# Kernel optimization log

Measured on AMD Instinct MI355X. Metric: run time of the kernel, lower is better.

The kernel has to match this reference:

```python
import jax, jax.numpy as jnp
import numpy as np

MACRO_CURVE_ORDER = 3
MAX_ACTION_LEN = 24
NUM_CURVES = 8
VOCAB = 361
NUM_LAYERS = 6
HID = 32


def setup_inputs() -> dict:
    key = jax.random.key(0)
    ks = iter(jax.random.split(key, 32))
    B, N_PART, P, CTX = 4096, 100, 64, 64

    def lin(k, din, dout):
        k1, k2 = jax.random.split(k)
        s = 1.0 / np.sqrt(din)
        return (jax.random.uniform(k1, (din, dout), jnp.float32, -s, s),
                jax.random.uniform(k2, (dout,), jnp.float32, -s, s))

    fc1_w, fc1_b = lin(next(ks), P, 256)
    fc2_w, fc2_b = lin(next(ks), 256, 256)
    fc3_w, fc3_b = lin(next(ks), CTX + 256, 512)
    fc4_w, fc4_b = lin(next(ks), 512, 256)
    fc5_w, fc5_b = lin(next(ks), 256, 128)
    fc6_w, fc6_b = lin(next(ks), 128, 32)
    fc10_w, fc10_b = lin(next(ks), HID, VOCAB)

    s = 1.0 / np.sqrt(HID)
    lstm_wih = jax.random.uniform(next(ks), (NUM_LAYERS, HID, 4 * HID), jnp.float32, -s, s)
    lstm_whh = jax.random.uniform(next(ks), (NUM_LAYERS, HID, 4 * HID), jnp.float32, -s, s)
    lstm_bih = jax.random.uniform(next(ks), (NUM_LAYERS, 4 * HID), jnp.float32, -s, s)
    lstm_bhh = jax.random.uniform(next(ks), (NUM_LAYERS, 4 * HID), jnp.float32, -s, s)

    return {
        "c": jax.random.normal(next(ks), (B, CTX), jnp.float32),
        "x": jax.random.normal(next(ks), (B, N_PART * P), jnp.float32),
        "hidden": jnp.zeros((NUM_LAYERS, B, HID), jnp.float32),
        "cell": jnp.zeros((NUM_LAYERS, B, HID), jnp.float32),
        "fc1_w": fc1_w, "fc1_b": fc1_b, "fc2_w": fc2_w, "fc2_b": fc2_b,
        "fc3_w": fc3_w, "fc3_b": fc3_b, "fc4_w": fc4_w, "fc4_b": fc4_b,
        "fc5_w": fc5_w, "fc5_b": fc5_b, "fc6_w": fc6_w, "fc6_b": fc6_b,
        "lstm_wih": lstm_wih, "lstm_whh": lstm_whh,
        "lstm_bih": lstm_bih, "lstm_bhh": lstm_bhh,
        "fc10_w": fc10_w, "fc10_b": fc10_b,
        "particle_size": P,
    }


def _lstm_stack(x, h, c, wih, whh, bih, bhh):
    """One time step through 6 stacked LSTM layers (PyTorch cell math)."""
    hs, cs = [], []
    inp = x
    for l in range(NUM_LAYERS):
        gates = inp @ wih[l] + bih[l] + h[l] @ whh[l] + bhh[l]  # (B, 4*HID)
        i, f, g, o = jnp.split(gates, 4, axis=-1)
        i, f, o = jax.nn.sigmoid(i), jax.nn.sigmoid(f), jax.nn.sigmoid(o)
        g = jnp.tanh(g)
        c_new = f * c[l] + i * g
        h_new = o * jnp.tanh(c_new)
        hs.append(h_new)
        cs.append(c_new)
        inp = h_new
    return inp, jnp.stack(hs), jnp.stack(cs)


def reference(c, x, hidden, cell, fc1_w, fc1_b, fc2_w, fc2_b, fc3_w, fc3_b,
              fc4_w, fc4_b, fc5_w, fc5_b, fc6_w, fc6_b,
              lstm_wih, lstm_whh, lstm_bih, lstm_bhh, fc10_w, fc10_b,
              particle_size):
    B = x.shape[0]
    # Belief (particle) encoder with mean pooling.
    xp = x.reshape(B, -1, particle_size)
    xp = jax.nn.relu(xp @ fc1_w + fc1_b)
    xp = jax.nn.relu(xp @ fc2_w + fc2_b)
    xp = xp.mean(axis=-2)  # (B, 256)
    z = jnp.concatenate([c, xp], axis=-1)
    z = jax.nn.relu(z @ fc3_w + fc3_b)
    z = jax.nn.relu(z @ fc4_w + fc4_b)
    z = jax.nn.relu(z @ fc5_w + fc5_b)
    z = jax.nn.relu(z @ fc6_w + fc6_b)  # (B, 32)

    def step(carry, _):
        xt, h, cst = carry
        xt, h, cst = _lstm_stack(xt, h, cst, lstm_wih, lstm_whh, lstm_bih, lstm_bhh)
        logits = xt @ fc10_w + fc10_b  # (B, VOCAB)
        idx = jax.lax.top_k(logits, NUM_CURVES)[1]  # (B, NUM_CURVES)
        return (xt, h, cst), idx

    (_, _, _), idxs = jax.lax.scan(step, (z, hidden, cell), None, length=MAX_ACTION_LEN)
    # (T, B, K) -> (B, T*K)
    preds = jnp.transpose(idxs, (1, 0, 2)).reshape(B, MAX_ACTION_LEN * NUM_CURVES)
    return preds
```

## Files before the change

### kernel.cpp

```cpp
#include <hip/hip_runtime.h>
#include <math.h>

#define BATCH 4096
#define NPART 100
#define PSZ   64

__device__ __forceinline__ void fma4(float4& d, const float s, const float4 v) {
    d.x = fmaf(s, v.x, d.x); d.y = fmaf(s, v.y, d.y);
    d.z = fmaf(s, v.z, d.z); d.w = fmaf(s, v.w, d.w);
}
__device__ __forceinline__ float4 addrelu4(const float4 a, const float4 b) {
    return make_float4(fmaxf(a.x + b.x, 0.f), fmaxf(a.y + b.y, 0.f),
                       fmaxf(a.z + b.z, 0.f), fmaxf(a.w + b.w, 0.f));
}

typedef const __attribute__((address_space(1))) unsigned int  gu32;
typedef __attribute__((address_space(3)))       unsigned int  lu32;
__device__ __forceinline__ void gload_lds16(const float* g, float* l) {
    __builtin_amdgcn_global_load_lds((gu32*)g, (lu32*)l, 16, 0, 0);
}

__device__ __forceinline__ void stage_panel(const float* __restrict__ w2,
                                            float* dst, const int p,
                                            const int wv, const int lane) {
    const float* g = w2 + p * (16 * 256) + wv * 256 + lane * 4;
    float*       l = dst + wv * 256;
    #pragma unroll
    for (int s = 0; s < 4; ++s)
        gload_lds16(g + s * 1024, l + s * 1024);
}

__global__ __launch_bounds__(256) void k_tw(
    const float* __restrict__ wih, const float* __restrict__ whh,
    const float* __restrict__ w10,
    float* __restrict__ wtih, float* __restrict__ wthh,
    float* __restrict__ w10t)
{
    const int i = blockIdx.x * 256 + threadIdx.x;
    if (i < 6 * 4096) {
        const int l = i >> 12, r = i & 4095;
        const int g = r >> 5,  k = r & 31;
        wtih[i] = wih[l * 4096 + k * 128 + g];
        wthh[i] = whh[l * 4096 + k * 128 + g];
    }
    if (i < 361 * 32) {
        const int v = i >> 5, k = i & 31;
        w10t[i] = w10[k * 361 + v];
    }
}

template<int NRR>
__device__ __forceinline__ void enc_chunk(
    const float* __restrict__ xb, const int rbase,
    const float* __restrict__ w1c, const float* __restrict__ w2,
    float* __restrict__ h1s, float* __restrict__ wpan,
    const int wv, const int lane, const int rg, const int col0,
    const float4 b1a, const float4 b1b, const float4 b2a, const float4 b2b,
    float* msum)
{
    stage_panel(w2, wpan, 0, wv, lane);

    int rowr[NRR];
    #pragma unroll
    for (int rr = 0; rr < NRR; ++rr)
        rowr[rr] = rbase + ((NRR == 1 && rg >= 4) ? 0 : (rg + 8 * rr));

    float4 a0[NRR], a1[NRR];
    #pragma unroll
    for (int rr = 0; rr < NRR; ++rr) {
        a0[rr] = make_float4(0.f, 0.f, 0.f, 0.f);
        a1[rr] = make_float4(0.f, 0.f, 0.f, 0.f);
    }
    #pragma unroll 2
    for (int k0 = 0; k0 < 64; k0 += 4) {
        float4 bva[4], bvb[4];
        #pragma unroll
        for (int kk = 0; kk < 4; ++kk) {
            bva[kk] = *(const float4*)(w1c + (k0 + kk) * 256);
            bvb[kk] = *(const float4*)(w1c + (k0 + kk) * 256 + 4);
        }
        #pragma unroll
        for (int rr = 0; rr < NRR; ++rr) {
            const float4 av = *(const float4*)(xb + (size_t)rowr[rr] * 64 + k0);
            fma4(a0[rr], av.x, bva[0]); fma4(a0[rr], av.y, bva[1]);
            fma4(a0[rr], av.z, bva[2]); fma4(a0[rr], av.w, bva[3]);
            fma4(a1[rr], av.x, bvb[0]); fma4(a1[rr], av.y, bvb[1]);
            fma4(a1[rr], av.z, bvb[2]); fma4(a1[rr], av.w, bvb[3]);
        }
    }
    #pragma unroll
    for (int rr = 0; rr < NRR; ++rr) {
        const int r = rg + 8 * rr;
        *(float4*)&h1s[r * 260 + col0]     = addrelu4(a0[rr], b1a);
        *(float4*)&h1s[r * 260 + col0 + 4] = addrelu4(a1[rr], b1b);
    }
    __syncthreads();

    float4 c0[NRR], c1[NRR];
    #pragma unroll
    for (int rr = 0; rr < NRR; ++rr) {
        c0[rr] = make_float4(0.f, 0.f, 0.f, 0.f);
        c1[rr] = make_float4(0.f, 0.f, 0.f, 0.f);
    }
    #pragma unroll 1
    for (int p = 0; p < 16; ++p) {
        if (p < 15)
            stage_panel(w2, wpan + ((p + 1) & 1) * (16 * 256), p + 1, wv, lane);
        const float* wp = wpan + (p & 1) * (16 * 256);
        #pragma unroll
        for (int it = 0; it < 4; ++it) {
            const int kk0 = it * 4;
            float4 bva[4], bvb[4];
            #pragma unroll
            for (int kk = 0; kk < 4; ++kk) {
                bva[kk] = *(const float4*)&wp[(kk0 + kk) * 256 + col0];
                bvb[kk] = *(const float4*)&wp[(kk0 + kk) * 256 + col0 + 4];
            }
            const int kg = p * 16 + kk0;
            #pragma unroll
            for (int rr = 0; rr < NRR; ++rr) {
                const float4 av = *(const float4*)&h1s[(rg + 8 * rr) * 260 + kg];
                fma4(c0[rr], av.x, bva[0]); fma4(c0[rr], av.y, bva[1]);
                fma4(c0[rr], av.z, bva[2]); fma4(c0[rr], av.w, bva[3]);
                fma4(c1[rr], av.x, bvb[0]); fma4(c1[rr], av.y, bvb[1]);
                fma4(c1[rr], av.z, bvb[2]); fma4(c1[rr], av.w, bvb[3]);
            }
        }
        __syncthreads();
    }

    #pragma unroll
    for (int rr = 0; rr < NRR; ++rr) {
        if (NRR == 4 || rg < 4) {
            msum[0] += fmaxf(c0[rr].x + b2a.x, 0.f);
            msum[1] += fmaxf(c0[rr].y + b2a.y, 0.f);
            msum[2] += fmaxf(c0[rr].z + b2a.z, 0.f);
            msum[3] += fmaxf(c0[rr].w + b2a.w, 0.f);
            msum[4] += fmaxf(c1[rr].x + b2b.x, 0.f);
            msum[5] += fmaxf(c1[rr].y + b2b.y, 0.f);
            msum[6] += fmaxf(c1[rr].z + b2b.z, 0.f);
            msum[7] += fmaxf(c1[rr].w + b2b.w, 0.f);
        }
    }
}

__global__ __launch_bounds__(256) void k_encoder(
    const float* __restrict__ x,
    const float* __restrict__ w1, const float* __restrict__ b1,
    const float* __restrict__ w2, const float* __restrict__ b2,
    float* __restrict__ xp)
{
    __shared__ __align__(16) float h1s[32 * 260];
    __shared__ __align__(16) float wpan[2 * 16 * 256];
    const int tid  = threadIdx.x;
    const int b    = blockIdx.x;
    const int lane = tid & 63;
    const int wv   = tid >> 6;
    const int cgw  = lane & 7;
    const int rg   = lane >> 3;
    const int col0 = wv * 64 + cgw * 8;

    const float* xb  = x + (size_t)b * (NPART * PSZ);
    const float* w1c = w1 + col0;
    const float4 b1a = *(const float4*)&b1[col0];
    const float4 b1b = *(const float4*)&b1[col0 + 4];
    const float4 b2a = *(const float4*)&b2[col0];
    const float4 b2b = *(const float4*)&b2[col0 + 4];

    float msum[8] = {0.f,0.f,0.f,0.f,0.f,0.f,0.f,0.f};

    enc_chunk<4>(xb,  0, w1c, w2, h1s, wpan, wv, lane, rg, col0, b1a, b1b, b2a, b2b, msum);
    enc_chunk<4>(xb, 32, w1c, w2, h1s, wpan, wv, lane, rg, col0, b1a, b1b, b2a, b2b, msum);
    enc_chunk<4>(xb, 64, w1c, w2, h1s, wpan, wv, lane, rg, col0, b1a, b1b, b2a, b2b, msum);
    enc_chunk<1>(xb, 96, w1c, w2, h1s, wpan, wv, lane, rg, col0, b1a, b1b, b2a, b2b, msum);

    #pragma unroll
    for (int q = 0; q < 8; ++q) {
        msum[q] += __shfl_xor(msum[q], 8, 64);
        msum[q] += __shfl_xor(msum[q], 16, 64);
        msum[q] += __shfl_xor(msum[q], 32, 64);
    }
    if (rg == 0) {
        float4 o0 = make_float4(msum[0] / 100.f, msum[1] / 100.f,
                                msum[2] / 100.f, msum[3] / 100.f);
        float4 o1 = make_float4(msum[4] / 100.f, msum[5] / 100.f,
                                msum[6] / 100.f, msum[7] / 100.f);
        *(float4*)&xp[(size_t)b * 256 + col0]     = o0;
        *(float4*)&xp[(size_t)b * 256 + col0 + 4] = o1;
    }
}

__global__ __launch_bounds__(256) void k_mlp(
    const float* __restrict__ cin, const float* __restrict__ xp,
    const float* __restrict__ w3, const float* __restrict__ b3,
    const float* __restrict__ w4, const float* __restrict__ b4,
    const float* __restrict__ w5, const float* __restrict__ b5,
    const float* __restrict__ w6, const float* __restrict__ b6,
    float* __restrict__ z)
{
    __shared__ float in0[8][320];
    __shared__ float h3[8][512];
    __shared__ float h4[8][256];
    __shared__ float h5[8][128];
    const int tid  = threadIdx.x;
    const int row0 = blockIdx.x * 8;

    for (int i = tid; i < 8 * 16; i += 256) {
        int r = i >> 4, q = i & 15;
        *(float4*)&in0[r][q * 4] = *(const float4*)&cin[(size_t)(row0 + r) * 64 + q * 4];
    }
    for (int i = tid; i < 8 * 64; i += 256) {
        int r = i >> 6, q = i & 63;
        *(float4*)&in0[r][64 + q * 4] = *(const float4*)&xp[(size_t)(row0 + r) * 256 + q * 4];
    }
    __syncthreads();

    {
        float a0[8], a1[8];
        #pragma unroll
        for (int r = 0; r < 8; ++r) { a0[r] = 0.f; a1[r] = 0.f; }
        const int c0 = tid, c1 = tid + 256;
        for (int kq = 0; kq < 80; ++kq) {
            const int k0 = kq * 4;
            float wa0 = w3[(k0+0)*512 + c0], wa1 = w3[(k0+1)*512 + c0];
            float wa2 = w3[(k0+2)*512 + c0], wa3 = w3[(k0+3)*512 + c0];
            float wb0 = w3[(k0+0)*512 + c1], wb1 = w3[(k0+1)*512 + c1];
            float wb2 = w3[(k0+2)*512 + c1], wb3 = w3[(k0+3)*512 + c1];
            #pragma unroll
            for (int r = 0; r < 8; ++r) {
                const float4 a = *(const float4*)&in0[r][k0];
                a0[r] = fmaf(a.x, wa0, fmaf(a.y, wa1, fmaf(a.z, wa2, fmaf(a.w, wa3, a0[r]))));
                a1[r] = fmaf(a.x, wb0, fmaf(a.y, wb1, fmaf(a.z, wb2, fmaf(a.w, wb3, a1[r]))));
            }
        }
        const float bb0 = b3[c0], bb1 = b3[c1];
        #pragma unroll
        for (int r = 0; r < 8; ++r) {
            h3[r][c0] = fmaxf(a0[r] + bb0, 0.f);
            h3[r][c1] = fmaxf(a1[r] + bb1, 0.f);
        }
    }
    __syncthreads();

    {
        float ac[8];
        #pragma unroll
        for (int r = 0; r < 8; ++r) ac[r] = 0.f;
        for (int kq = 0; kq < 128; ++kq) {
            const int k0 = kq * 4;
            float w0 = w4[(k0+0)*256 + tid], w1v = w4[(k0+1)*256 + tid];
            float w2v = w4[(k0+2)*256 + tid], w3v = w4[(k0+3)*256 + tid];
            #pragma unroll
            for (int r = 0; r < 8; ++r) {
                const float4 a = *(const float4*)&h3[r][k0];
                ac[r] = fmaf(a.x, w0, fmaf(a.y, w1v, fmaf(a.z, w2v, fmaf(a.w, w3v, ac[r]))));
            }
        }
        const float bb = b4[tid];
        #pragma unroll
        for (int r = 0; r < 8; ++r) h4[r][tid] = fmaxf(ac[r] + bb, 0.f);
    }
    __syncthreads();

    {
        const int c5 = tid & 127, half = tid >> 7;
        float ac[4];
        #pragma unroll
        for (int r = 0; r < 4; ++r) ac[r] = 0.f;
        for (int kq = 0; kq < 64; ++kq) {
            const int k0 = kq * 4;
            float w0 = w5[(k0+0)*128 + c5], w1v = w5[(k0+1)*128 + c5];
            float w2v = w5[(k0+2)*128 + c5], w3v = w5[(k0+3)*128 + c5];
            #pragma unroll
            for (int r = 0; r < 4; ++r) {
                const float4 a = *(const float4*)&h4[half * 4 + r][k0];
                ac[r] = fmaf(a.x, w0, fmaf(a.y, w1v, fmaf(a.z, w2v, fmaf(a.w, w3v, ac[r]))));
            }
        }
        const float bb = b5[c5];
        #pragma unroll
        for (int r = 0; r < 4; ++r) h5[half * 4 + r][c5] = fmaxf(ac[r] + bb, 0.f);
    }
    __syncthreads();

    {
        const int c6 = tid & 31, r = tid >> 5;
        float ac = 0.f;
        for (int kq = 0; kq < 32; ++kq) {
            const int k0 = kq * 4;
            float w0 = w6[(k0+0)*32 + c6], w1v = w6[(k0+1)*32 + c6];
            float w2v = w6[(k0+2)*32 + c6], w3v = w6[(k0+3)*32 + c6];
            const float4 a = *(const float4*)&h5[r][k0];
            ac = fmaf(a.x, w0, fmaf(a.y, w1v, fmaf(a.z, w2v, fmaf(a.w, w3v, ac))));
        }
        z[(size_t)(row0 + r) * 32 + c6] = fmaxf(ac + b6[c6], 0.f);
    }
}

__global__ __launch_bounds__(256) void k_lstm(
    const float* __restrict__ z,
    const float* __restrict__ hid0, const float* __restrict__ cel0,
    const float* __restrict__ wtih, const float* __restrict__ wthh,
    const float* __restrict__ bih, const float* __restrict__ bhh,
    const float* __restrict__ w10t, const float* __restrict__ b10,
    int* __restrict__ out)
{
    __shared__ float xs[8][32];
    __shared__ float hs[6][8][32];
    __shared__ float cs[6][8][32];
    __shared__ float gates[8][128];
    __shared__ float logits[8][361];
    const int tid  = threadIdx.x;
    const int row0 = blockIdx.x * 8;

    for (int i = tid; i < 8 * 32; i += 256) xs[0][i] = z[(size_t)row0 * 32 + i];
    for (int i = tid; i < 6 * 8 * 32; i += 256) {
        int l = i >> 8, rj = i & 255;
        (&hs[0][0][0])[i] = hid0[(size_t)l * BATCH * 32 + (size_t)row0 * 32 + rj];
        (&cs[0][0][0])[i] = cel0[(size_t)l * BATCH * 32 + (size_t)row0 * 32 + rj];
    }
    __syncthreads();

    const int g  = tid & 127, rg = tid >> 7;
    const int jc = tid & 31,  jr = tid >> 5;
    const int wv = tid >> 6,  lane = tid & 63;

    for (int t = 0; t < 24; ++t) {
        for (int l = 0; l < 6; ++l) {
            const float* inp = (l == 0) ? ((t == 0) ? &xs[0][0] : &hs[5][0][0])
                                        : &hs[l - 1][0][0];
            const float* WIt = wtih + (size_t)l * 4096 + g * 32;
            const float* WHt = wthh + (size_t)l * 4096 + g * 32;
            const float bsum = bih[l * 128 + g] + bhh[l * 128 + g];
            float acc[4] = {bsum, bsum, bsum, bsum};
            #pragma unroll
            for (int k = 0; k < 32; k += 4) {
                const float4 wi = *(const float4*)&WIt[k];
                const float4 wh = *(const float4*)&WHt[k];
                #pragma unroll
                for (int rr = 0; rr < 4; ++rr) {
                    const int r = rg * 4 + rr;
                    const float4 ai = *(const float4*)&inp[r * 32 + k];
                    const float4 ah = *(const float4*)&hs[l][r][k];
                    acc[rr] = fmaf(ai.x, wi.x, acc[rr]); acc[rr] = fmaf(ai.y, wi.y, acc[rr]);
                    acc[rr] = fmaf(ai.z, wi.z, acc[rr]); acc[rr] = fmaf(ai.w, wi.w, acc[rr]);
                    acc[rr] = fmaf(ah.x, wh.x, acc[rr]); acc[rr] = fmaf(ah.y, wh.y, acc[rr]);
                    acc[rr] = fmaf(ah.z, wh.z, acc[rr]); acc[rr] = fmaf(ah.w, wh.w, acc[rr]);
                }
            }
            #pragma unroll
            for (int rr = 0; rr < 4; ++rr) gates[rg * 4 + rr][g] = acc[rr];
            __syncthreads();

            {
                const float gi = gates[jr][jc],      gf = gates[jr][32 + jc];
                const float gg = gates[jr][64 + jc], go = gates[jr][96 + jc];
                const float i_ = 1.f / (1.f + expf(-gi));
                const float f_ = 1.f / (1.f + expf(-gf));
                const float o_ = 1.f / (1.f + expf(-go));
                const float g_ = tanhf(gg);
                const float cn = f_ * cs[l][jr][jc] + i_ * g_;
                cs[l][jr][jc] = cn;
                hs[l][jr][jc] = o_ * tanhf(cn);
            }
            __syncthreads();
        }

        #pragma unroll
        for (int pass = 0; pass < 2; ++pass) {
            const int v = tid + pass * 256;
            if (v < 361) {
                const float bb = b10[v];
                const float* wv4 = w10t + v * 32;
                float a8[8];
                #pragma unroll
                for (int r = 0; r < 8; ++r) a8[r] = bb;
                #pragma unroll
                for (int k = 0; k < 32; k += 4) {
                    const float4 w4v = *(const float4*)&wv4[k];
                    #pragma unroll
                    for (int r = 0; r < 8; ++r) {
                        const float4 a = *(const float4*)&hs[5][r][k];
                        a8[r] = fmaf(a.x, w4v.x, fmaf(a.y, w4v.y, fmaf(a.z, w4v.z, fmaf(a.w, w4v.w, a8[r]))));
                    }
                }
                #pragma unroll
                for (int r = 0; r < 8; ++r) logits[r][v] = a8[r];
            }
        }
        __syncthreads();

        for (int rr = 0; rr < 2; ++rr) {
            const int r = wv * 2 + rr;
            float val[6];
            #pragma unroll
            for (int s = 0; s < 6; ++s) {
                const int v = lane + 64 * s;
                val[s] = (v < 361) ? logits[r][v] : -3.4e38f;
            }
            unsigned msk = 0x3Fu;
            const int rowg = row0 + r;
            for (int sel = 0; sel < 8; ++sel) {
                float bv = -3.4e38f; int bi = 0x7FFFFFFF;
                #pragma unroll
                for (int s = 0; s < 6; ++s) {
                    if (msk & (1u << s)) {
                        const float v2 = val[s]; const int i2 = lane + 64 * s;
                        if (v2 > bv || (v2 == bv && i2 < bi)) { bv = v2; bi = i2; }
                    }
                }
                #pragma unroll
                for (int off = 32; off >= 1; off >>= 1) {
                    const float ov = __shfl_xor(bv, off, 64);
                    const int   oi = __shfl_xor(bi, off, 64);
                    if (ov > bv || (ov == bv && oi < bi)) { bv = ov; bi = oi; }
                }
                if ((bi & 63) == lane) msk &= ~(1u << (bi >> 6));
                if (lane == 0) out[(size_t)rowg * 192 + t * 8 + sel] = bi;
            }
        }
        __syncthreads();
    }
}

extern "C" void kernel_launch(void* const* d_in, const int* in_sizes, int n_in,
                              void* d_out, int out_size, void* d_ws, size_t ws_size,
                              hipStream_t stream) {
    const float* cin  = (const float*)d_in[0];
    const float* x    = (const float*)d_in[1];
    const float* hid0 = (const float*)d_in[2];
    const float* cel0 = (const float*)d_in[3];
    const float* w1 = (const float*)d_in[4];  const float* b1 = (const float*)d_in[5];
    const float* w2 = (const float*)d_in[6];  const float* b2 = (const float*)d_in[7];
    const float* w3 = (const float*)d_in[8];  const float* b3 = (const float*)d_in[9];
    const float* w4 = (const float*)d_in[10]; const float* b4 = (const float*)d_in[11];
    const float* w5 = (const float*)d_in[12]; const float* b5 = (const float*)d_in[13];
    const float* w6 = (const float*)d_in[14]; const float* b6 = (const float*)d_in[15];
    const float* wih = (const float*)d_in[16]; const float* whh = (const float*)d_in[17];
    const float* bih = (const float*)d_in[18]; const float* bhh = (const float*)d_in[19];
    const float* w10 = (const float*)d_in[20]; const float* b10 = (const float*)d_in[21];

    float* xp   = (float*)d_ws;
    float* zz   = xp + (size_t)BATCH * 256;
    float* wtih = zz + (size_t)BATCH * 32;
    float* wthh = wtih + 6 * 4096;
    float* w10t = wthh + 6 * 4096;
    int*   out  = (int*)d_out;

    k_tw<<<96, 256, 0, stream>>>(wih, whh, w10, wtih, wthh, w10t);
    k_encoder<<<BATCH, 256, 0, stream>>>(x, w1, b1, w2, b2, xp);
    k_mlp<<<BATCH / 8, 256, 0, stream>>>(cin, xp, w3, b3, w4, b4, w5, b5, w6, b6, zz);
    k_lstm<<<BATCH / 8, 256, 0, stream>>>(zz, hid0, cel0, wtih, wthh, bih, bhh, w10t, b10, out);
}
```

Before: 2.234 ms.

## Make each wave own two LSTM rows and replace block barriers with wave barriers

The LSTM/top-k kernel is repartitioned so each 64-lane wave handles two batch rows end to end: all 128 gates, the cell update, the 361 logits and the top-8 selection. Every cross-wave __syncthreads in the 24x6 recurrence is replaced with a wave-level barrier, removing block-wide synchronisation from the serial critical path. In exchange, each wave now does more weight loads and FMAs per row pair, with less reuse of weights across rows. Correctness depends on LDS writes being visible within the wave without a block barrier.

```diff
diff --git a/kernel.cpp b/kernel.cpp
--- a/kernel.cpp
+++ b/kernel.cpp
@@ -8,6 +8,10 @@
 __device__ __forceinline__ void fma4(float4& d, const float s, const float4 v) {
     d.x = fmaf(s, v.x, d.x); d.y = fmaf(s, v.y, d.y);
     d.z = fmaf(s, v.z, d.z); d.w = fmaf(s, v.w, d.w);
+}
+__device__ __forceinline__ float dot4(const float4 a, const float4 b, float acc) {
+    acc = fmaf(a.x, b.x, acc); acc = fmaf(a.y, b.y, acc);
+    acc = fmaf(a.z, b.z, acc); return fmaf(a.w, b.w, acc);
 }
 __device__ __forceinline__ float4 addrelu4(const float4 a, const float4 b) {
     return make_float4(fmaxf(a.x + b.x, 0.f), fmaxf(a.y + b.y, 0.f),
@@ -311,46 +315,55 @@
     __shared__ float gates[8][128];
     __shared__ float logits[8][361];
     const int tid  = threadIdx.x;
+    const int lane = tid & 63;
+    const int wv   = tid >> 6;
     const int row0 = blockIdx.x * 8;
-
-    for (int i = tid; i < 8 * 32; i += 256) xs[0][i] = z[(size_t)row0 * 32 + i];
-    for (int i = tid; i < 6 * 8 * 32; i += 256) {
-        int l = i >> 8, rj = i & 255;
-        (&hs[0][0][0])[i] = hid0[(size_t)l * BATCH * 32 + (size_t)row0 * 32 + rj];
-        (&cs[0][0][0])[i] = cel0[(size_t)l * BATCH * 32 + (size_t)row0 * 32 + rj];
-    }
-    __syncthreads();
-
-    const int g  = tid & 127, rg = tid >> 7;
-    const int jc = tid & 31,  jr = tid >> 5;
-    const int wv = tid >> 6,  lane = tid & 63;
+    const int r0   = wv * 2, r1 = r0 + 1;
+
+    {
+        const int rr = lane >> 5, j = lane & 31;
+        const int gr = row0 + r0 + rr;
+        xs[r0 + rr][j] = z[(size_t)gr * 32 + j];
+        #pragma unroll
+        for (int l = 0; l < 6; ++l) {
+            hs[l][r0 + rr][j] = hid0[(size_t)l * BATCH * 32 + (size_t)gr * 32 + j];
+            cs[l][r0 + rr][j] = cel0[(size_t)l * BATCH * 32 + (size_t)gr * 32 + j];
+        }
+    }
+    __builtin_amdgcn_wave_barrier();
+
+    const int cA = lane, cB = lane + 64;
+    const int jr = r0 + (lane >> 5), jc = lane & 31;
 
     for (int t = 0; t < 24; ++t) {
         for (int l = 0; l < 6; ++l) {
-            const float* inp = (l == 0) ? ((t == 0) ? &xs[0][0] : &hs[5][0][0])
-                                        : &hs[l - 1][0][0];
-            const float* WIt = wtih + (size_t)l * 4096 + g * 32;
-            const float* WHt = wthh + (size_t)l * 4096 + g * 32;
-            const float bsum = bih[l * 128 + g] + bhh[l * 128 + g];
-            float acc[4] = {bsum, bsum, bsum, bsum};
+            const float* inp = (l == 0) ? ((t == 0) ? &xs[r0][0] : &hs[5][r0][0])
+                                        : &hs[l - 1][r0][0];
+            const float* WAi = wtih + (size_t)l * 4096 + cA * 32;
+            const float* WAh = wthh + (size_t)l * 4096 + cA * 32;
+            const float* WBi = wtih + (size_t)l * 4096 + cB * 32;
+            const float* WBh = wthh + (size_t)l * 4096 + cB * 32;
+            const float bA = bih[l * 128 + cA] + bhh[l * 128 + cA];
+            const float bB = bih[l * 128 + cB] + bhh[l * 128 + cB];
+            float aA0 = bA, aA1 = bA, aB0 = bB, aB1 = bB;
             #pragma unroll
             for (int k = 0; k < 32; k += 4) {
-                const float4 wi = *(const float4*)&WIt[k];
-                const float4 wh = *(const float4*)&WHt[k];
-                #pragma unroll
-                for (int rr = 0; rr < 4; ++rr) {
-                    const int r = rg * 4 + rr;
-                    const float4 ai = *(const float4*)&inp[r * 32 + k];
-                    const float4 ah = *(const float4*)&hs[l][r][k];
-                    acc[rr] = fmaf(ai.x, wi.x, acc[rr]); acc[rr] = fmaf(ai.y, wi.y, acc[rr]);
-                    acc[rr] = fmaf(ai.z, wi.z, acc[rr]); acc[rr] = fmaf(ai.w, wi.w, acc[rr]);
-                    acc[rr] = fmaf(ah.x, wh.x, acc[rr]); acc[rr] = fmaf(ah.y, wh.y, acc[rr]);
-                    acc[rr] = fmaf(ah.z, wh.z, acc[rr]); acc[rr] = fmaf(ah.w, wh.w, acc[rr]);
-                }
-            }
-            #pragma unroll
-            for (int rr = 0; rr < 4; ++rr) gates[rg * 4 + rr][g] = acc[rr];
-            __syncthreads();
+                const float4 wiA = *(const float4*)&WAi[k];
+                const float4 whA = *(const float4*)&WAh[k];
+                const float4 wiB = *(const float4*)&WBi[k];
+                const float4 whB = *(const float4*)&WBh[k];
+                const float4 x0 = *(const float4*)&inp[k];
+                const float4 x1 = *(const float4*)&inp[32 + k];
+                const float4 h0 = *(const float4*)&hs[l][r0][k];
+                const float4 h1 = *(const float4*)&hs[l][r1][k];
+                aA0 = dot4(x0, wiA, aA0); aA0 = dot4(h0, whA, aA0);
+                aA1 = dot4(x1, wiA, aA1); aA1 = dot4(h1, whA, aA1);
+                aB0 = dot4(x0, wiB, aB0); aB0 = dot4(h0, whB, aB0);
+                aB1 = dot4(x1, wiB, aB1); aB1 = dot4(h1, whB, aB1);
+            }
+            gates[r0][cA] = aA0; gates[r1][cA] = aA1;
+            gates[r0][cB] = aB0; gates[r1][cB] = aB1;
+            __builtin_amdgcn_wave_barrier();
 
             {
                 const float gi = gates[jr][jc],      gf = gates[jr][32 + jc];
@@ -363,35 +376,33 @@
                 cs[l][jr][jc] = cn;
                 hs[l][jr][jc] = o_ * tanhf(cn);
             }
-            __syncthreads();
-        }
-
-        #pragma unroll
-        for (int pass = 0; pass < 2; ++pass) {
-            const int v = tid + pass * 256;
+            __builtin_amdgcn_wave_barrier();
+        }
+
+        #pragma unroll
+        for (int s = 0; s < 6; ++s) {
+            const int v = lane + 64 * s;
             if (v < 361) {
                 const float bb = b10[v];
                 const float* wv4 = w10t + v * 32;
-                float a8[8];
-                #pragma unroll
-                for (int r = 0; r < 8; ++r) a8[r] = bb;
+                float p0 = bb, p1 = bb;
                 #pragma unroll
                 for (int k = 0; k < 32; k += 4) {
                     const float4 w4v = *(const float4*)&wv4[k];
-                    #pragma unroll
-                    for (int r = 0; r < 8; ++r) {
-                        const float4 a = *(const float4*)&hs[5][r][k];
-                        a8[r] = fmaf(a.x, w4v.x, fmaf(a.y, w4v.y, fmaf(a.z, w4v.z, fmaf(a.w, w4v.w, a8[r]))));
-                    }
+                    const float4 a0 = *(const float4*)&hs[5][r0][k];
+                    const float4 a1 = *(const float4*)&hs[5][r1][k];
+                    p0 = dot4(a0, w4v, p0);
+                    p1 = dot4(a1, w4v, p1);
                 }
-                #pragma unroll
-                for (int r = 0; r < 8; ++r) logits[r][v] = a8[r];
-            }
-        }
-        __syncthreads();
-
+                logits[r0][v] = p0;
+                logits[r1][v] = p1;
+            }
+        }
+        __builtin_amdgcn_wave_barrier();
+
+        #pragma unroll 1
         for (int rr = 0; rr < 2; ++rr) {
-            const int r = wv * 2 + rr;
+            const int r = r0 + rr;
             float val[6];
             #pragma unroll
             for (int s = 0; s < 6; ++s) {
@@ -419,7 +430,7 @@
                 if (lane == 0) out[(size_t)rowg * 192 + t * 8 + sel] = bi;
             }
         }
-        __syncthreads();
+        __builtin_amdgcn_wave_barrier();
     }
 }
 
```

New measurement: 3.035 ms. 35.9% more time.
